# Performance work log

Hardware: AMD Instinct MI355X
Metric: run time of the kernel (lower is better)

Reference implementation:

```python
import jax, jax.numpy as jnp
import numpy as np
import math

B, S, D = 32, 2048, 1024


def setup_inputs() -> dict:
    key = jax.random.key(0)
    ks = jax.random.split(key, 8)
    x = jax.random.normal(ks[0], (B, S, D), dtype=jnp.float32)
    # right-padding mask: True = padding, each row has a random valid length in [S//2, S]
    lengths = jax.random.randint(ks[1], (B, 1), S // 2, S + 1)
    attention_mask = jnp.arange(S)[None, :] >= lengths  # [B, S] bool
    scale = 1.0 / math.sqrt(D)
    gate_w1 = jax.random.normal(ks[2], (D, D // 2), dtype=jnp.float32) * scale
    gate_b1 = jnp.zeros((D // 2,), dtype=jnp.float32)
    gate_w2 = jax.random.normal(ks[3], (D // 2, 1), dtype=jnp.float32) * scale
    gate_b2 = jnp.zeros((1,), dtype=jnp.float32)
    decay_lambda = jnp.float32(0.05)
    attention_query = jax.random.normal(ks[4], (D,), dtype=jnp.float32)
    key_w = jax.random.normal(ks[5], (D, D), dtype=jnp.float32) * scale
    key_b = jnp.zeros((D,), dtype=jnp.float32)
    return {
        "utterance_embeddings": x,
        "attention_mask": attention_mask,
        "gate_w1": gate_w1, "gate_b1": gate_b1,
        "gate_w2": gate_w2, "gate_b2": gate_b2,
        "decay_lambda": decay_lambda,
        "attention_query": attention_query,
        "key_w": key_w, "key_b": key_b,
    }


def reference(utterance_embeddings, attention_mask, gate_w1, gate_b1, gate_w2,
              gate_b2, decay_lambda, attention_query, key_w, key_b):
    x = utterance_embeddings  # [B, S, D]
    bsz, seq_len, dim = x.shape
    # suppression gate: Linear -> GELU(exact) -> Linear -> Sigmoid, output [B, S, 1]
    h = jax.nn.gelu(jnp.einsum('bsd,dk->bsk', x, gate_w1) + gate_b1, approximate=False)
    gate = jax.nn.sigmoid(jnp.einsum('bsk,ko->bso', h, gate_w2) + gate_b2)
    gated = x * gate  # [B, S, D]
    keys = jnp.einsum('bsd,de->bse', gated, key_w) + key_b  # [B, S, D]
    logits = jnp.einsum('d,bsd->bs', attention_query, keys) / jnp.sqrt(jnp.float32(dim))
    t_idx = jnp.arange(seq_len, dtype=jnp.float32)[None, :]  # [1, S]
    valid_lengths = jnp.sum(~attention_mask, axis=1, keepdims=True).astype(jnp.float32)
    penalty_idx = jnp.maximum(valid_lengths - 1.0 - t_idx, 0.0)  # [B, S]
    pos_lambda = jax.nn.softplus(decay_lambda)
    decayed = logits - pos_lambda * penalty_idx
    decayed = jnp.where(attention_mask, jnp.float32(-10000.0), decayed)
    alpha = jax.nn.softmax(decayed, axis=1)  # [B, S]
    scene_vector = jnp.einsum('bs,bsd->bd', alpha, gated)  # [B, D]
    return scene_vector
```

## Files before the change

kernel.cpp:

```cpp
#include <hip/hip_runtime.h>
#include <hip/hip_bf16.h>
#include <math.h>

#define BQ 32
#define SQ 2048
#define DQ 1024
#define NQ 512
#define MQ (BQ*SQ)
#define BM 128
#define BN 256
#define BK 32

typedef __attribute__((ext_vector_type(8))) short bf16x8;
typedef __attribute__((ext_vector_type(4))) float f32x4;

__device__ __forceinline__ short f2bf(float f){
  return __builtin_bit_cast(short, __float2bfloat16(f));
}

__device__ __forceinline__ void gload_lds16(const void* g, void* l){
  __builtin_amdgcn_global_load_lds(
      (const __attribute__((address_space(1))) unsigned int*)g,
      (__attribute__((address_space(3))) unsigned int*)l, 16, 0, 0);
}

__global__ void k_det(const uint4* __restrict__ m, int* __restrict__ flag){
  __shared__ int so, sf;
  int t = threadIdx.x;
  if (t==0){ so=0; sf=0; }
  __syncthreads();
  int o=0, f1=0;
  #pragma unroll 4
  for (int i=t;i<MQ/16;i+=256){
    uint4 v = m[i];
    if (v.x==0x3F800000u||v.y==0x3F800000u||v.z==0x3F800000u||v.w==0x3F800000u) f1=1;
    else if (v.x>1u||v.y>1u||v.z>1u||v.w>1u) o=1;
  }
  if (o) atomicOr(&so,1);
  if (f1) atomicOr(&sf,1);
  __syncthreads();
  if (t==0) *flag = so?2:(sf?1:0);
}

__global__ __launch_bounds__(256) void k_prep(
    const float* __restrict__ w1, short* __restrict__ w1t,
    const float* __restrict__ kw, const float* __restrict__ kb,
    const float* __restrict__ q, float* __restrict__ wq,
    const void* __restrict__ maskp, const int* __restrict__ flag,
    int* __restrict__ lens)
{
  __shared__ float tile[64][65];
  int blk = blockIdx.x, t = threadIdx.x;
  if (blk < 128){
    int kt = blk >> 3, nt = blk & 7;
    int c = t & 63, rq = t >> 6;
    #pragma unroll
    for (int i=0;i<16;i++){
      int r = rq + i*4;
      tile[r][c] = w1[(size_t)(kt*64 + r)*NQ + nt*64 + c];
    }
    __syncthreads();
    #pragma unroll
    for (int i=0;i<16;i++){
      int nr = rq + i*4;
      w1t[(size_t)(nt*64 + nr)*DQ + kt*64 + c] = f2bf(tile[c][nr]);
    }
  } else if (blk < 1153){
    int d = blk - 128;
    const float* row = (d < DQ) ? (kw + (size_t)d*DQ) : kb;
    float s = 0.f;
    for (int e=t;e<DQ;e+=256) s += row[e]*q[e];
    #pragma unroll
    for (int o=32;o;o>>=1) s += __shfl_down(s,o);
    if ((t&63)==0) tile[0][t>>6]=s;
    __syncthreads();
    if (t==0) wq[d] = tile[0][0]+tile[0][1]+tile[0][2]+tile[0][3];
  } else {
    int b = blk - 1153;
    int fl = *flag;
    const unsigned char* m8 = (const unsigned char*)maskp;
    const float* mf = (const float*)maskp;
    const int* mi = (const int*)maskp;
    int cnt = 0;
    #pragma unroll
    for (int i=0;i<8;i++){
      size_t idx = (size_t)b*SQ + t + i*256;
      int mm = (fl==2) ? (m8[idx]!=0) : (fl==1) ? (mf[idx]!=0.0f) : (mi[idx]!=0);
      cnt += mm^1;
    }
    #pragma unroll
    for (int o=32;o;o>>=1) cnt += __shfl_down(cnt,o);
    if ((t&63)==0) tile[0][t>>6]=(float)cnt;
    __syncthreads();
    if (t==0) lens[b] = (int)(tile[0][0]+tile[0][1]+tile[0][2]+tile[0][3]);
  }
}

__global__ __launch_bounds__(512) void k_gate(
    const float* __restrict__ x, const short* __restrict__ w1t,
    const float* __restrict__ wq, const float* __restrict__ w2,
    const float* __restrict__ b1,
    float* __restrict__ gpart, float* __restrict__ xq)
{
  __shared__ __align__(16) short As[2][BM*BK];
  __shared__ __align__(16) short Bs[2][BN*BK];
  __shared__ float wqs[DQ];

  int tid = threadIdx.x;
  int phys = blockIdx.x;
  int bid = ((phys & 7) << 7) | (phys >> 3);
  int bm = bid >> 1, bn = bid & 1;
  int m0 = bm*BM;
  int lane = tid & 63, wid = tid >> 6;
  int wm = wid >> 2, wn = wid & 3;
  int lo = lane & 15, hi = lane >> 4;

  wqs[tid]     = wq[tid];
  wqs[tid+512] = wq[tid+512];

  int ar = tid >> 2, ac = (tid & 3) * 8;
  const float* asrc = x + (size_t)(m0 + ar)*DQ + ac;
  const short* bsrc = w1t + (size_t)(bn*BN + (tid>>2))*DQ + (tid&3)*8;

  float w2v[4], b1v[4];
  #pragma unroll
  for (int fn=0;fn<4;fn++){
    int n = bn*BN + wn*64 + fn*16 + lo;
    w2v[fn] = w2[n]; b1v[fn] = b1[n];
  }

  f32x4 r0 = *(const f32x4*)(asrc);
  f32x4 r1 = *(const f32x4*)(asrc + 4);
  gload_lds16(bsrc,                    &Bs[0][tid*8]);
  gload_lds16(bsrc + (size_t)128*DQ,   &Bs[0][tid*8 + 4096]);
  __syncthreads();
  float xqacc = 0.f;
  {
    if (bn == 0){
      f32x4 w0 = *(const f32x4*)(wqs + ac);
      f32x4 w1v = *(const f32x4*)(wqs + ac + 4);
      #pragma unroll
      for (int j=0;j<4;j++)
        xqacc += r0[j]*w0[j] + r1[j]*w1v[j];
    }
    bf16x8 s0;
    #pragma unroll
    for (int j=0;j<4;j++){ s0[j]=f2bf(r0[j]); s0[4+j]=f2bf(r1[j]); }
    *(bf16x8*)(&As[0][ar*BK + ac]) = s0;
  }
  __syncthreads();

  f32x4 acc[4][4];
  #pragma unroll
  for (int a=0;a<4;a++)
    #pragma unroll
    for (int b=0;b<4;b++) acc[a][b] = (f32x4){0.f,0.f,0.f,0.f};

  for (int t=0;t<32;t++){
    int cur = t & 1, nxt = cur ^ 1;
    int k0n = (t+1)*BK;
    if (t < 31){
      r0 = *(const f32x4*)(asrc + k0n);
      r1 = *(const f32x4*)(asrc + k0n + 4);
      gload_lds16(bsrc + k0n,                  &Bs[nxt][tid*8]);
      gload_lds16(bsrc + (size_t)128*DQ + k0n, &Bs[nxt][tid*8 + 4096]);
    }
    bf16x8 af[4], bfr[4];
    #pragma unroll
    for (int fm=0;fm<4;fm++)
      af[fm] = *(const bf16x8*)(&As[cur][(wm*64+fm*16+lo)*BK + hi*8]);
    #pragma unroll
    for (int fn=0;fn<4;fn++)
      bfr[fn] = *(const bf16x8*)(&Bs[cur][(wn*64+fn*16+lo)*BK + hi*8]);
    #pragma unroll
    for (int fm=0;fm<4;fm++)
      #pragma unroll
      for (int fn=0;fn<4;fn++)
        acc[fm][fn] = __builtin_amdgcn_mfma_f32_16x16x32_bf16(af[fm], bfr[fn], acc[fm][fn], 0,0,0);
    if (t < 31){
      if (bn == 0){
        f32x4 w0 = *(const f32x4*)(wqs + k0n + ac);
        f32x4 w1v = *(const f32x4*)(wqs + k0n + ac + 4);
        #pragma unroll
        for (int j=0;j<4;j++)
          xqacc += r0[j]*w0[j] + r1[j]*w1v[j];
      }
      bf16x8 s0;
      #pragma unroll
      for (int j=0;j<4;j++){ s0[j]=f2bf(r0[j]); s0[4+j]=f2bf(r1[j]); }
      *(bf16x8*)(&As[nxt][ar*BK + ac]) = s0;
    }
    __syncthreads();
  }

  if (bn == 0){
    float s = xqacc;
    s += __shfl_xor(s, 1);
    s += __shfl_xor(s, 2);
    if ((tid & 3) == 0) xq[m0 + ar] = s;
  }

  #pragma unroll
  for (int fm=0;fm<4;fm++){
    #pragma unroll
    for (int j=0;j<4;j++){
      float s = 0.f;
      #pragma unroll
      for (int fn=0;fn<4;fn++){
        float h = acc[fm][fn][j] + b1v[fn];
        float g = 0.5f*h*(1.0f + erff(h*0.70710678118f));
        s += g*w2v[fn];
      }
      s += __shfl_xor(s,1); s += __shfl_xor(s,2);
      s += __shfl_xor(s,4); s += __shfl_xor(s,8);
      if (lo == 0){
        int p = bn*4 + wn;
        gpart[(size_t)p*MQ + m0 + wm*64 + fm*16 + hi*4 + j] = s;
      }
    }
  }
}

__global__ __launch_bounds__(256) void k_wpool(
    const float* __restrict__ x, const float* __restrict__ gpart,
    const float* __restrict__ xqv, const float* __restrict__ wq,
    const float* __restrict__ b2p, const float* __restrict__ lamp,
    const void* __restrict__ maskp, const int* __restrict__ flag,
    const int* __restrict__ lens,
    float* __restrict__ part, float* __restrict__ wsumv)
{
  __shared__ float wrow[64];
  int blk = blockIdx.x, t = threadIdx.x;
  int batch = blk >> 5;
  int sBase = (blk & 31) * 64;
  size_t R0 = (size_t)blk * 64;
  if (t < 64){
    size_t r = R0 + t;
    float gsum = b2p[0];
    #pragma unroll
    for (int p=0;p<8;p++) gsum += gpart[(size_t)p*MQ + r];
    float gate = 1.0f/(1.0f+expf(-gsum));
    float qb = wq[DQ];
    float lg = (gate*xqv[r] + qb)*0.03125f;
    float lam = lamp[0];
    float posl = fmaxf(lam,0.f) + log1pf(expf(-fabsf(lam)));
    int L = lens[batch];
    int s = sBase + t;
    float pen = fmaxf((float)L - 1.0f - (float)s, 0.0f);
    int fl = *flag;
    size_t mi_ = (size_t)batch*SQ + s;
    int mm = (fl==2) ? (((const unsigned char*)maskp)[mi_]!=0)
           : (fl==1) ? (((const float*)maskp)[mi_]!=0.0f)
                     : (((const int*)maskp)[mi_]!=0);
    float e = mm ? 0.0f : expf(lg - posl*pen);
    wrow[t] = e*gate;
    float ts = e;
    #pragma unroll
    for (int o=1;o<64;o<<=1) ts += __shfl_xor(ts,o);
    if (t==0) wsumv[blk] = ts;
  }
  __syncthreads();

  int d0 = t*4;
  const float* xb = x + R0*DQ + d0;
  f32x4 a = {0.f,0.f,0.f,0.f};
  #pragma unroll 8
  for (int s=0;s<64;s++){
    float w = wrow[s];
    f32x4 v = *(const f32x4*)(xb + (size_t)s*DQ);
    a[0] += w*v[0]; a[1] += w*v[1]; a[2] += w*v[2]; a[3] += w*v[3];
  }
  *(f32x4*)(part + (size_t)blk*DQ + d0) = a;
}

__global__ __launch_bounds__(256) void k_fin(const float* __restrict__ part,
                                             const float* __restrict__ wsumv,
                                             float* __restrict__ out){
  int i = blockIdx.x*256 + threadIdx.x;
  int b = i >> 10, d = i & 1023;
  float den = 0.f;
  #pragma unroll
  for (int c=0;c<32;c++) den += wsumv[b*32+c];
  float s = 0.f;
  #pragma unroll
  for (int c=0;c<32;c++) s += part[((size_t)(b*32+c))*DQ + d];
  out[i] = s/den;
}

extern "C" void kernel_launch(void* const* d_in, const int* in_sizes, int n_in,
                              void* d_out, int out_size, void* d_ws, size_t ws_size,
                              hipStream_t stream)
{
  const float* x    = (const float*)d_in[0];
  const void*  mask = d_in[1];
  const float* w1   = (const float*)d_in[2];
  const float* b1   = (const float*)d_in[3];
  const float* w2   = (const float*)d_in[4];
  const float* b2   = (const float*)d_in[5];
  const float* lam  = (const float*)d_in[6];
  const float* q    = (const float*)d_in[7];
  const float* kw   = (const float*)d_in[8];
  const float* kb   = (const float*)d_in[9];
  char* ws = (char*)d_ws;
  short* w1t   = (short*)ws;
  float* wq    = (float*)(ws + (1<<20));
  int*   flag  = (int*)(ws + (1<<20) + 8192);
  int*   lens  = (int*)(ws + (1<<20) + 8448);
  float* wsumv = (float*)(ws + (1<<20) + 12544);
  float* xqv   = (float*)(ws + (1<<20) + 32768);
  float* gpart = (float*)(ws + (2<<20));
  float* part  = (float*)(ws + (4<<20));
  float* out   = (float*)d_out;

  k_det<<<dim3(1), 256, 0, stream>>>((const uint4*)mask, flag);
  k_prep<<<dim3(1185), 256, 0, stream>>>(w1, w1t, kw, kb, q, wq,
                                         mask, flag, lens);
  k_gate<<<dim3((MQ/BM)*(NQ/BN)), 512, 0, stream>>>(x, w1t, wq, w2, b1,
                                                    gpart, xqv);
  k_wpool<<<dim3(MQ/64), 256, 0, stream>>>(x, gpart, xqv, wq, b2, lam,
                                           mask, flag, lens, part, wsumv);
  k_fin<<<dim3((BQ*DQ)/256), 256, 0, stream>>>(part, wsumv, out);
}
```

Before: 170.6 us.

## Enlarge gate GEMM tiles to 256x256x64 with XOR-swizzled LDS layout

Doubles the M tile and the K step of the gate GEMM, so each workgroup computes 256x256 outputs with an 8x4 MFMA fragment grid per wave. This halves the number of K iterations and barriers and increases reuse of each loaded W1 tile. A and B tiles in LDS now use an XOR chunk swizzle to avoid bank conflicts on the 64-wide rows. The cost is much more LDS per block (about 128KB) and twice the accumulator registers, which lowers occupancy and risks spills under the new launch bound.

Result: slower. 225.5 us (+32.2%).

```diff
diff --git a/kernel.cpp b/kernel.cpp
--- a/kernel.cpp
+++ b/kernel.cpp
@@ -7,9 +7,9 @@
 #define DQ 1024
 #define NQ 512
 #define MQ (BQ*SQ)
-#define BM 128
+#define BM 256
 #define BN 256
-#define BK 32
+#define BK 64
 
 typedef __attribute__((ext_vector_type(8))) short bf16x8;
 typedef __attribute__((ext_vector_type(4))) float f32x4;
@@ -96,7 +96,7 @@
   }
 }
 
-__global__ __launch_bounds__(512) void k_gate(
+__global__ __launch_bounds__(512, 2) void k_gate(
     const float* __restrict__ x, const short* __restrict__ w1t,
     const float* __restrict__ wq, const float* __restrict__ w2,
     const float* __restrict__ b1,
@@ -108,100 +108,116 @@
 
   int tid = threadIdx.x;
   int phys = blockIdx.x;
-  int bid = ((phys & 7) << 7) | (phys >> 3);
+  int bid = ((phys & 7) << 6) | (phys >> 3);
   int bm = bid >> 1, bn = bid & 1;
-  int m0 = bm*BM;
+  int m0 = bm*BM, n0 = bn*BN;
   int lane = tid & 63, wid = tid >> 6;
   int wm = wid >> 2, wn = wid & 3;
   int lo = lane & 15, hi = lane >> 4;
+  int lo7 = lo & 7;
+
+  int arow = tid >> 1;
+  int ah   = (tid & 1) * 32;
+  int ac0  = (tid & 1) * 4;
+  int arow7 = arow & 7;
+  const float* abase = x + (size_t)(m0 + arow)*DQ + ah;
+  int brow = tid >> 3;
+  int bchunk = (tid & 7) ^ (brow & 7);
+  const short* bbase = w1t + (size_t)(n0 + brow)*DQ + bchunk*8;
+
+  float w2v[4], b1v[4];
+  #pragma unroll
+  for (int fn=0;fn<4;fn++){
+    int n = n0 + wn*64 + fn*16 + lo;
+    w2v[fn] = w2[n]; b1v[fn] = b1[n];
+  }
 
   wqs[tid]     = wq[tid];
   wqs[tid+512] = wq[tid+512];
-
-  int ar = tid >> 2, ac = (tid & 3) * 8;
-  const float* asrc = x + (size_t)(m0 + ar)*DQ + ac;
-  const short* bsrc = w1t + (size_t)(bn*BN + (tid>>2))*DQ + (tid&3)*8;
-
-  float w2v[4], b1v[4];
-  #pragma unroll
-  for (int fn=0;fn<4;fn++){
-    int n = bn*BN + wn*64 + fn*16 + lo;
-    w2v[fn] = w2[n]; b1v[fn] = b1[n];
-  }
-
-  f32x4 r0 = *(const f32x4*)(asrc);
-  f32x4 r1 = *(const f32x4*)(asrc + 4);
-  gload_lds16(bsrc,                    &Bs[0][tid*8]);
-  gload_lds16(bsrc + (size_t)128*DQ,   &Bs[0][tid*8 + 4096]);
+  f32x4 a[8];
+  #pragma unroll
+  for (int j=0;j<8;j++) a[j] = *(const f32x4*)(abase + 4*j);
+  #pragma unroll
+  for (int i=0;i<4;i++)
+    gload_lds16(bbase + (size_t)(i*64)*DQ, &Bs[0][i*4096 + tid*8]);
   __syncthreads();
   float xqacc = 0.f;
-  {
-    if (bn == 0){
-      f32x4 w0 = *(const f32x4*)(wqs + ac);
-      f32x4 w1v = *(const f32x4*)(wqs + ac + 4);
-      #pragma unroll
-      for (int j=0;j<4;j++)
-        xqacc += r0[j]*w0[j] + r1[j]*w1v[j];
-    }
-    bf16x8 s0;
-    #pragma unroll
-    for (int j=0;j<4;j++){ s0[j]=f2bf(r0[j]); s0[4+j]=f2bf(r1[j]); }
-    *(bf16x8*)(&As[0][ar*BK + ac]) = s0;
-  }
-  __syncthreads();
-
-  f32x4 acc[4][4];
-  #pragma unroll
-  for (int a=0;a<4;a++)
-    #pragma unroll
-    for (int b=0;b<4;b++) acc[a][b] = (f32x4){0.f,0.f,0.f,0.f};
-
-  for (int t=0;t<32;t++){
+  if (bn == 0){
+    #pragma unroll
+    for (int j=0;j<8;j++){
+      f32x4 w = *(const f32x4*)(wqs + ah + 4*j);
+      xqacc += a[j][0]*w[0] + a[j][1]*w[1] + a[j][2]*w[2] + a[j][3]*w[3];
+    }
+  }
+  #pragma unroll
+  for (int j=0;j<4;j++){
+    bf16x8 sv;
+    #pragma unroll
+    for (int e=0;e<4;e++){ sv[e]=f2bf(a[2*j][e]); sv[4+e]=f2bf(a[2*j+1][e]); }
+    *(bf16x8*)(&As[0][arow*64 + (((ac0+j) ^ arow7)<<3)]) = sv;
+  }
+  __syncthreads();
+
+  f32x4 acc[8][4];
+  #pragma unroll
+  for (int i=0;i<8;i++)
+    #pragma unroll
+    for (int jj=0;jj<4;jj++) acc[i][jj] = (f32x4){0.f,0.f,0.f,0.f};
+
+  for (int t=0; t<16; ++t){
     int cur = t & 1, nxt = cur ^ 1;
-    int k0n = (t+1)*BK;
-    if (t < 31){
-      r0 = *(const f32x4*)(asrc + k0n);
-      r1 = *(const f32x4*)(asrc + k0n + 4);
-      gload_lds16(bsrc + k0n,                  &Bs[nxt][tid*8]);
-      gload_lds16(bsrc + (size_t)128*DQ + k0n, &Bs[nxt][tid*8 + 4096]);
-    }
-    bf16x8 af[4], bfr[4];
-    #pragma unroll
-    for (int fm=0;fm<4;fm++)
-      af[fm] = *(const bf16x8*)(&As[cur][(wm*64+fm*16+lo)*BK + hi*8]);
-    #pragma unroll
-    for (int fn=0;fn<4;fn++)
-      bfr[fn] = *(const bf16x8*)(&Bs[cur][(wn*64+fn*16+lo)*BK + hi*8]);
-    #pragma unroll
-    for (int fm=0;fm<4;fm++)
-      #pragma unroll
-      for (int fn=0;fn<4;fn++)
-        acc[fm][fn] = __builtin_amdgcn_mfma_f32_16x16x32_bf16(af[fm], bfr[fn], acc[fm][fn], 0,0,0);
-    if (t < 31){
+    int k1 = (t+1)*BK;
+    if (t < 15){
+      #pragma unroll
+      for (int j=0;j<8;j++) a[j] = *(const f32x4*)(abase + k1 + 4*j);
+      #pragma unroll
+      for (int i=0;i<4;i++)
+        gload_lds16(bbase + (size_t)(i*64)*DQ + k1, &Bs[nxt][i*4096 + tid*8]);
+    }
+    #pragma unroll
+    for (int ks=0; ks<2; ++ks){
+      bf16x8 bfr[4];
+      #pragma unroll
+      for (int fn=0;fn<4;fn++){
+        int r = wn*64 + fn*16 + lo;
+        bfr[fn] = *(const bf16x8*)(&Bs[cur][r*64 + (((ks*4+hi) ^ lo7)<<3)]);
+      }
+      #pragma unroll
+      for (int fm=0;fm<8;fm++){
+        int r = wm*128 + fm*16 + lo;
+        bf16x8 af = *(const bf16x8*)(&As[cur][r*64 + (((ks*4+hi) ^ lo7)<<3)]);
+        #pragma unroll
+        for (int fn=0;fn<4;fn++)
+          acc[fm][fn] = __builtin_amdgcn_mfma_f32_16x16x32_bf16(af, bfr[fn], acc[fm][fn], 0,0,0);
+      }
+    }
+    if (t < 15){
       if (bn == 0){
-        f32x4 w0 = *(const f32x4*)(wqs + k0n + ac);
-        f32x4 w1v = *(const f32x4*)(wqs + k0n + ac + 4);
         #pragma unroll
-        for (int j=0;j<4;j++)
-          xqacc += r0[j]*w0[j] + r1[j]*w1v[j];
-      }
-      bf16x8 s0;
-      #pragma unroll
-      for (int j=0;j<4;j++){ s0[j]=f2bf(r0[j]); s0[4+j]=f2bf(r1[j]); }
-      *(bf16x8*)(&As[nxt][ar*BK + ac]) = s0;
-    }
-    __syncthreads();
+        for (int j=0;j<8;j++){
+          f32x4 w = *(const f32x4*)(wqs + k1 + ah + 4*j);
+          xqacc += a[j][0]*w[0] + a[j][1]*w[1] + a[j][2]*w[2] + a[j][3]*w[3];
+        }
+      }
+      #pragma unroll
+      for (int j=0;j<4;j++){
+        bf16x8 sv;
+        #pragma unroll
+        for (int e=0;e<4;e++){ sv[e]=f2bf(a[2*j][e]); sv[4+e]=f2bf(a[2*j+1][e]); }
+        *(bf16x8*)(&As[nxt][arow*64 + (((ac0+j) ^ arow7)<<3)]) = sv;
+      }
+      __syncthreads();
+    }
   }
 
   if (bn == 0){
     float s = xqacc;
     s += __shfl_xor(s, 1);
-    s += __shfl_xor(s, 2);
-    if ((tid & 3) == 0) xq[m0 + ar] = s;
-  }
-
-  #pragma unroll
-  for (int fm=0;fm<4;fm++){
+    if ((tid & 1) == 0) xq[m0 + arow] = s;
+  }
+
+  #pragma unroll
+  for (int fm=0;fm<8;fm++){
     #pragma unroll
     for (int j=0;j<4;j++){
       float s = 0.f;
@@ -215,7 +231,7 @@
       s += __shfl_xor(s,4); s += __shfl_xor(s,8);
       if (lo == 0){
         int p = bn*4 + wn;
-        gpart[(size_t)p*MQ + m0 + wm*64 + fm*16 + hi*4 + j] = s;
+        gpart[(size_t)p*MQ + m0 + wm*128 + fm*16 + hi*4 + j] = s;
       }
     }
   }
@@ -263,14 +279,14 @@
 
   int d0 = t*4;
   const float* xb = x + R0*DQ + d0;
-  f32x4 a = {0.f,0.f,0.f,0.f};
+  f32x4 aa = {0.f,0.f,0.f,0.f};
   #pragma unroll 8
   for (int s=0;s<64;s++){
     float w = wrow[s];
     f32x4 v = *(const f32x4*)(xb + (size_t)s*DQ);
-    a[0] += w*v[0]; a[1] += w*v[1]; a[2] += w*v[2]; a[3] += w*v[3];
-  }
-  *(f32x4*)(part + (size_t)blk*DQ + d0) = a;
+    aa[0] += w*v[0]; aa[1] += w*v[1]; aa[2] += w*v[2]; aa[3] += w*v[3];
+  }
+  *(f32x4*)(part + (size_t)blk*DQ + d0) = aa;
 }
 
 __global__ __launch_bounds__(256) void k_fin(const float* __restrict__ part,
```
